# Optimization experiments

Measured on AMD Instinct MI355X. Metric: run time of the kernel, lower is better.

The kernel has to match this reference:

```python
import jax, jax.numpy as jnp
import numpy as np

N, E, D = 20000, 320000, 256
EPS = 1e-5


def setup_inputs() -> dict:
    key = jax.random.key(0)
    ks = jax.random.split(key, 12)
    s = 1.0 / np.sqrt(D)
    s2 = 1.0 / np.sqrt(2 * D)
    return {
        "node_embeddings": jax.random.normal(ks[0], (N, D), jnp.float32),
        "edge_index": jax.random.randint(ks[1], (2, E), 0, N, jnp.int64),
        "edge_embeddings": jax.random.normal(ks[2], (E, D), jnp.float32),
        # message MLP: Linear(D,D) -> GELU -> Linear(D,D)
        "W1m": jax.random.uniform(ks[3], (D, D), jnp.float32, -s, s),
        "b1m": jnp.zeros((D,), jnp.float32),
        "W2m": jax.random.uniform(ks[4], (D, D), jnp.float32, -s, s),
        "b2m": jnp.zeros((D,), jnp.float32),
        # update MLP: Linear(D,2D) -> GELU -> Linear(2D,D)
        "W1u": jax.random.uniform(ks[5], (D, 2 * D), jnp.float32, -s, s),
        "b1u": jnp.zeros((2 * D,), jnp.float32),
        "W2u": jax.random.uniform(ks[6], (2 * D, D), jnp.float32, -s2, s2),
        "b2u": jnp.zeros((D,), jnp.float32),
        # LayerNorm params
        "gamma": jnp.ones((D,), jnp.float32),
        "beta": jnp.zeros((D,), jnp.float32),
    }


def _layer_norm(x, gamma, beta):
    mu = jnp.mean(x, axis=-1, keepdims=True)
    var = jnp.mean(jnp.square(x - mu), axis=-1, keepdims=True)
    return (x - mu) * jax.lax.rsqrt(var + EPS) * gamma + beta


def reference(node_embeddings, edge_index, edge_embeddings,
              W1m, b1m, W2m, b2m, W1u, b1u, W2u, b2u, gamma, beta):
    src = edge_index[0]
    dst = edge_index[1]
    n = node_embeddings.shape[0]
    # gather + edge add + message MLP (exact erf GELU, as torch default)
    h = node_embeddings[src] + edge_embeddings           # [E, D]
    h = jax.nn.gelu(h @ W1m + b1m, approximate=False)
    messages = h @ W2m + b2m                             # [E, D]
    # scatter-mean aggregation
    agg = jax.ops.segment_sum(messages, dst, num_segments=n)  # [N, D]
    deg = jax.ops.segment_sum(jnp.ones((dst.shape[0], 1), node_embeddings.dtype),
                              dst, num_segments=n)            # [N, 1]
    agg = agg / jnp.maximum(deg, 1.0)
    # update MLP + residual + LayerNorm
    u = jax.nn.gelu(agg @ W1u + b1u, approximate=False) @ W2u + b2u
    return _layer_norm(node_embeddings + u, gamma, beta)
```

## Files before the change

kernel.cpp:

```cpp
#include <hip/hip_runtime.h>
#include <hip/hip_bf16.h>

#define N_NODES 20000
#define N_EDGES 320000
#define EBLK 32
#define NBLK 32

typedef __attribute__((ext_vector_type(8))) short short8;
typedef __attribute__((ext_vector_type(4))) float f32x4;

static __device__ __forceinline__ unsigned short f2bf(float f) {
  __hip_bfloat16 h = __float2bfloat16(f);
  union { __hip_bfloat16 h; unsigned short u; } cv; cv.h = h; return cv.u;
}

static __device__ __forceinline__ unsigned int pk2(float a, float b) {
  return (unsigned int)f2bf(a) | ((unsigned int)f2bf(b) << 16);
}

static __device__ __forceinline__ float gelu_f(float x) {
  float z = x * (2.3022082f + 0.1029432f * x * x);
  z = fminf(fmaxf(z, -30.0f), 30.0f);
  float t = exp2f(z);
  return x * t * __frcp_rn(1.0f + t);
}

#define SWZ(row, byteoff) ((byteoff) ^ (((row) & 7) << 4))
#define SWZU(b) ((b) ^ ((((b) >> 8) & 7) << 4))

__global__ void zero_kernel(float4* __restrict__ S4, int4* __restrict__ cnt4) {
  int idx = blockIdx.x * blockDim.x + threadIdx.x;
  S4[idx] = make_float4(0.f, 0.f, 0.f, 0.f);
  if (idx < N_NODES / 4) cnt4[idx] = make_int4(0, 0, 0, 0);
}

__global__ void pack_kernel(const float* __restrict__ W1m, const float* __restrict__ W2m,
                            const float* __restrict__ W1u, const float* __restrict__ W2u,
                            unsigned short* __restrict__ P1m, unsigned short* __restrict__ P2m,
                            unsigned short* __restrict__ P1u, unsigned short* __restrict__ P2u) {
  int idx = blockIdx.x * blockDim.x + threadIdx.x;
  const float* W; unsigned short* P; int K, Nc, local;
  if (idx < 65536)        { W = W1m; P = P1m; K = 256; Nc = 256; local = idx; }
  else if (idx < 131072)  { W = W2m; P = P2m; K = 256; Nc = 256; local = idx - 65536; }
  else if (idx < 262144)  { W = W1u; P = P1u; K = 256; Nc = 512; local = idx - 131072; }
  else                    { W = W2u; P = P2u; K = 512; Nc = 256; local = idx - 262144; }
  int frag = local >> 9, wi = local & 511;
  int l = wi >> 3, i = wi & 7;
  int kf = K >> 5;
  int cf = frag / kf, t = frag % kf;
  int k = t * 32 + (l >> 4) * 8 + i;
  int n = cf * 16 + (l & 15);
  P[local] = f2bf(W[(size_t)k * Nc + n]);
}

__global__ void hist_kernel(const int* __restrict__ dst, int* __restrict__ cnt) {
  int e = blockIdx.x * blockDim.x + threadIdx.x;
  atomicAdd(&cnt[dst[e]], 1);
}

__global__ __launch_bounds__(1024) void scan_kernel(const int* __restrict__ cnt,
                                                    int* __restrict__ rptr,
                                                    int* __restrict__ cur) {
  __shared__ int sums[1024];
  const int t = threadIdx.x;
  const int base = t * 20;
  int local[20];
  int s = 0;
#pragma unroll
  for (int i = 0; i < 20; ++i) {
    int idx = base + i;
    int v = (idx < N_NODES) ? cnt[idx] : 0;
    local[i] = s;
    s += v;
  }
  int v = s;
  sums[t] = v;
  for (int off = 1; off < 1024; off <<= 1) {
    __syncthreads();
    int o = (t >= off) ? sums[t - off] : 0;
    __syncthreads();
    v += o;
    sums[t] = v;
  }
  int excl = v - s;
#pragma unroll
  for (int i = 0; i < 20; ++i) {
    int idx = base + i;
    if (idx < N_NODES) { int p = excl + local[i]; rptr[idx] = p; cur[idx] = p; }
  }
  if (t == 1023) rptr[N_NODES] = v;
}

__global__ void scatter_kernel(const int* __restrict__ dst, int* __restrict__ cur,
                               int* __restrict__ perm) {
  int e = blockIdx.x * blockDim.x + threadIdx.x;
  int d = dst[e];
  int pos = atomicAdd(&cur[d], 1);
  perm[pos] = e;
}

__global__ __launch_bounds__(256, 8) void edge_kernel(
    const float* __restrict__ node, const float* __restrict__ eemb,
    const int* __restrict__ src, const int* __restrict__ dst,
    const int* __restrict__ perm,
    const unsigned short* __restrict__ P1m, const float* __restrict__ b1m,
    float* __restrict__ S) {
  __shared__ unsigned short tA[EBLK * 256];
  __shared__ int dstS[EBLK];
  const int tid = threadIdx.x;
  const int e0 = blockIdx.x * EBLK;
  {
    const int r = tid >> 3;
    const int cs = (tid & 7) * 32;
    const int e = perm[e0 + r];
    const int se = src[e];
    if ((tid & 7) == 0) dstS[r] = dst[e];
    const float* ep = eemb + (size_t)e * 256 + cs;
    const float* np = node + (size_t)se * 256 + cs;
#pragma unroll
    for (int i = 0; i < 4; ++i) {
      float4 a = *(const float4*)(ep + i * 8);
      float4 b = *(const float4*)(np + i * 8);
      float4 c = *(const float4*)(ep + i * 8 + 4);
      float4 d = *(const float4*)(np + i * 8 + 4);
      uint4 p;
      p.x = pk2(a.x + b.x, a.y + b.y);
      p.y = pk2(a.z + b.z, a.w + b.w);
      p.z = pk2(c.x + d.x, c.y + d.y);
      p.w = pk2(c.z + d.z, c.w + d.w);
      *(uint4*)((char*)tA + SWZ(r, r * 512 + (cs + i * 8) * 2)) = p;
    }
  }
  __syncthreads();

  const int w = tid >> 6, l = tid & 63;
  const int lr = l & 15, lh = l >> 4;
  f32x4 acc[2][4];
#pragma unroll
  for (int c = 0; c < 4; ++c) {
    float bb = b1m[w * 64 + c * 16 + lr];
    acc[0][c] = f32x4{bb, bb, bb, bb};
    acc[1][c] = f32x4{bb, bb, bb, bb};
  }
#pragma unroll
  for (int kt = 0; kt < 8; ++kt) {
    const int row0 = lr, row1 = 16 + lr;
    short8 af0 = *(const short8*)((const char*)tA + SWZ(row0, row0 * 512 + kt * 64 + lh * 16));
    short8 af1 = *(const short8*)((const char*)tA + SWZ(row1, row1 * 512 + kt * 64 + lh * 16));
#pragma unroll
    for (int c = 0; c < 4; ++c) {
      short8 bfr = *(const short8*)(P1m + (size_t)(((w * 4 + c) * 8 + kt) * 512 + l * 8));
      acc[0][c] = __builtin_amdgcn_mfma_f32_16x16x32_bf16(af0, bfr, acc[0][c], 0, 0, 0);
      acc[1][c] = __builtin_amdgcn_mfma_f32_16x16x32_bf16(af1, bfr, acc[1][c], 0, 0, 0);
    }
  }

#pragma unroll
  for (int r4 = 0; r4 < 2; ++r4)
#pragma unroll
    for (int c = 0; c < 4; ++c)
#pragma unroll
      for (int j = 0; j < 4; ++j)
        acc[r4][c][j] = gelu_f(acc[r4][c][j]);

  const int dv = dstS[l & 31];
  const int pv = __shfl(dv, (l - 1) & 63);
  const bool bflag = (l < 32) && ((l == 0) || (dv != pv));
  const unsigned long long mask = __ballot(bflag);
  const int nseg = __popcll(mask);
  int sid[2][4];
#pragma unroll
  for (int r4 = 0; r4 < 2; ++r4)
#pragma unroll
    for (int j = 0; j < 4; ++j) {
      int row = r4 * 16 + lh * 4 + j;
      sid[r4][j] = __popcll(mask & ((2ULL << row) - 1)) - 1;
    }
  unsigned long long rem = mask;
  for (int s = 0; s < nseg; ++s) {
    const int rowf = __builtin_ctzll(rem);
    rem &= rem - 1;
    const int dseg = __shfl(dv, rowf);
    float p0 = 0.f, p1 = 0.f, p2 = 0.f, p3 = 0.f;
#pragma unroll
    for (int r4 = 0; r4 < 2; ++r4)
#pragma unroll
      for (int j = 0; j < 4; ++j) {
        bool m = (sid[r4][j] == s);
        p0 += m ? acc[r4][0][j] : 0.f;
        p1 += m ? acc[r4][1][j] : 0.f;
        p2 += m ? acc[r4][2][j] : 0.f;
        p3 += m ? acc[r4][3][j] : 0.f;
      }
    p0 += __shfl_xor(p0, 16); p0 += __shfl_xor(p0, 32);
    p1 += __shfl_xor(p1, 16); p1 += __shfl_xor(p1, 32);
    p2 += __shfl_xor(p2, 16); p2 += __shfl_xor(p2, 32);
    p3 += __shfl_xor(p3, 16); p3 += __shfl_xor(p3, 32);
    if (lh == 0) {
      float* Sp = S + (size_t)dseg * 256 + w * 64 + lr;
      atomicAdd(Sp, p0);
      atomicAdd(Sp + 16, p1);
      atomicAdd(Sp + 32, p2);
      atomicAdd(Sp + 48, p3);
    }
  }
}

__global__ __launch_bounds__(256, 4) void node_kernel(
    const float* __restrict__ node, const float* __restrict__ S, const int* __restrict__ rptr,
    const unsigned short* __restrict__ P2m, const float* __restrict__ b2m,
    const unsigned short* __restrict__ P1u, const float* __restrict__ b1u,
    const unsigned short* __restrict__ P2u, const float* __restrict__ b2u,
    const float* __restrict__ gamma, const float* __restrict__ beta,
    float* __restrict__ out) {
  __shared__ unsigned short tAB[2][NBLK * 256];
  __shared__ unsigned short tH[NBLK * 256];
  __shared__ float fmu[NBLK], frs[NBLK], fflag[NBLK];
  float* tU = (float*)tAB;
  const int tid = threadIdx.x;
  const int n0 = blockIdx.x * NBLK;
  const int r = tid >> 3;
  const int cs = (tid & 7) * 32;
  const int n = n0 + r;
  {
    int dgi = rptr[n + 1] - rptr[n];
    float rec = 1.0f / fmaxf((float)dgi, 1.0f);
    if ((tid & 7) == 0) fflag[r] = (dgi > 0) ? 1.0f : 0.0f;
    const float* sp = S + (size_t)n * 256 + cs;
#pragma unroll
    for (int i = 0; i < 4; ++i) {
      float4 a = *(const float4*)(sp + i * 8);
      float4 b = *(const float4*)(sp + i * 8 + 4);
      uint4 p;
      p.x = pk2(a.x * rec, a.y * rec);
      p.y = pk2(a.z * rec, a.w * rec);
      p.z = pk2(b.x * rec, b.y * rec);
      p.w = pk2(b.z * rec, b.w * rec);
      *(uint4*)((char*)tAB[0] + SWZ(r, r * 512 + (cs + i * 8) * 2)) = p;
    }
  }
  __syncthreads();
  const int w = tid >> 6, l = tid & 63, lr = l & 15, lh = l >> 4;

  {
    f32x4 acc[2][4];
#pragma unroll
    for (int r4 = 0; r4 < 2; ++r4)
#pragma unroll
      for (int c = 0; c < 4; ++c) acc[r4][c] = f32x4{0.f, 0.f, 0.f, 0.f};
#pragma unroll
    for (int t = 0; t < 8; ++t) {
      const int row0 = lr, row1 = 16 + lr;
      short8 af0 = *(const short8*)((const char*)tAB[0] + SWZ(row0, row0 * 512 + t * 64 + lh * 16));
      short8 af1 = *(const short8*)((const char*)tAB[0] + SWZ(row1, row1 * 512 + t * 64 + lh * 16));
#pragma unroll
      for (int c = 0; c < 4; ++c) {
        short8 bfr = *(const short8*)(P2m + (size_t)(((w * 4 + c) * 8 + t) * 512 + l * 8));
        acc[0][c] = __builtin_amdgcn_mfma_f32_16x16x32_bf16(af0, bfr, acc[0][c], 0, 0, 0);
        acc[1][c] = __builtin_amdgcn_mfma_f32_16x16x32_bf16(af1, bfr, acc[1][c], 0, 0, 0);
      }
    }
#pragma unroll
    for (int r4 = 0; r4 < 2; ++r4)
#pragma unroll
      for (int c = 0; c < 4; ++c) {
        int col = w * 64 + c * 16 + lr;
        float bm = b2m[col];
#pragma unroll
        for (int j = 0; j < 4; ++j) {
          int row = r4 * 16 + lh * 4 + j;
          float v = acc[r4][c][j] + fflag[row] * bm;
          *(unsigned short*)((char*)tAB[1] + SWZ(row, row * 512 + col * 2)) = f2bf(v);
        }
      }
  }
  __syncthreads();

  f32x4 acc3[2][4];
#pragma unroll
  for (int c = 0; c < 4; ++c) {
    float bb = b2u[w * 64 + c * 16 + lr];
    acc3[0][c] = f32x4{bb, bb, bb, bb};
    acc3[1][c] = f32x4{bb, bb, bb, bb};
  }
#pragma unroll
  for (int half = 0; half < 2; ++half) {
    {
      f32x4 acc[2][4];
#pragma unroll
      for (int r4 = 0; r4 < 2; ++r4)
#pragma unroll
        for (int c = 0; c < 4; ++c) acc[r4][c] = f32x4{0.f, 0.f, 0.f, 0.f};
#pragma unroll
      for (int t = 0; t < 8; ++t) {
        const int row0 = lr, row1 = 16 + lr;
        short8 af0 = *(const short8*)((const char*)tAB[1] + SWZ(row0, row0 * 512 + t * 64 + lh * 16));
        short8 af1 = *(const short8*)((const char*)tAB[1] + SWZ(row1, row1 * 512 + t * 64 + lh * 16));
#pragma unroll
        for (int c = 0; c < 4; ++c) {
          short8 bfr = *(const short8*)(P1u + (size_t)(((half * 16 + w * 4 + c) * 8 + t) * 512 + l * 8));
          acc[0][c] = __builtin_amdgcn_mfma_f32_16x16x32_bf16(af0, bfr, acc[0][c], 0, 0, 0);
          acc[1][c] = __builtin_amdgcn_mfma_f32_16x16x32_bf16(af1, bfr, acc[1][c], 0, 0, 0);
        }
      }
#pragma unroll
      for (int r4 = 0; r4 < 2; ++r4)
#pragma unroll
        for (int c = 0; c < 4; ++c) {
          int col = w * 64 + c * 16 + lr;
          float b1 = b1u[half * 256 + col];
#pragma unroll
          for (int j = 0; j < 4; ++j) {
            int row = r4 * 16 + lh * 4 + j;
            float v = gelu_f(acc[r4][c][j] + b1);
            *(unsigned short*)((char*)tH + SWZ(row, row * 512 + col * 2)) = f2bf(v);
          }
        }
    }
    __syncthreads();
    {
#pragma unroll
      for (int tt = 0; tt < 8; ++tt) {
        const int row0 = lr, row1 = 16 + lr;
        short8 af0 = *(const short8*)((const char*)tH + SWZ(row0, row0 * 512 + tt * 64 + lh * 16));
        short8 af1 = *(const short8*)((const char*)tH + SWZ(row1, row1 * 512 + tt * 64 + lh * 16));
#pragma unroll
        for (int c = 0; c < 4; ++c) {
          short8 bfr = *(const short8*)(P2u + (size_t)(((w * 4 + c) * 16 + half * 8 + tt) * 512 + l * 8));
          acc3[0][c] = __builtin_amdgcn_mfma_f32_16x16x32_bf16(af0, bfr, acc3[0][c], 0, 0, 0);
          acc3[1][c] = __builtin_amdgcn_mfma_f32_16x16x32_bf16(af1, bfr, acc3[1][c], 0, 0, 0);
        }
      }
    }
    __syncthreads();
  }

#pragma unroll
  for (int r4 = 0; r4 < 2; ++r4)
#pragma unroll
    for (int c = 0; c < 4; ++c) {
      int col = w * 64 + c * 16 + lr;
#pragma unroll
      for (int j = 0; j < 4; ++j) {
        int row = r4 * 16 + lh * 4 + j;
        *(float*)((char*)tU + SWZU(row * 1024 + col * 4)) = acc3[r4][c][j];
      }
    }
  __syncthreads();

  {
    float sum = 0.f, sq = 0.f;
#pragma unroll
    for (int i = 0; i < 8; ++i) {
      int byte = SWZU(r * 1024 + (cs + i * 4) * 4);
      float4 v = *(float4*)((char*)tU + byte);
      const float4 nb = *(const float4*)(node + (size_t)n * 256 + cs + i * 4);
      v.x += nb.x; v.y += nb.y; v.z += nb.z; v.w += nb.w;
      *(float4*)((char*)tU + byte) = v;
      sum += v.x + v.y + v.z + v.w;
      sq += v.x * v.x + v.y * v.y + v.z * v.z + v.w * v.w;
    }
    sum += __shfl_xor(sum, 1); sum += __shfl_xor(sum, 2); sum += __shfl_xor(sum, 4);
    sq  += __shfl_xor(sq, 1);  sq  += __shfl_xor(sq, 2);  sq  += __shfl_xor(sq, 4);
    if ((tid & 7) == 0) {
      float mu = sum * (1.0f / 256.0f);
      fmu[r] = mu;
      frs[r] = rsqrtf(fmaxf(sq * (1.0f / 256.0f) - mu * mu, 0.0f) + 1e-5f);
    }
  }
  __syncthreads();
#pragma unroll
  for (int i = 0; i < 8; ++i) {
    int f4 = i * 256 + tid;
    int row = f4 >> 6;
    int c4 = f4 & 63;
    float4 v = *(float4*)((char*)tU + SWZU(row * 1024 + c4 * 16));
    float mu = fmu[row], rs = frs[row];
    float4 g  = *(const float4*)(gamma + c4 * 4);
    float4 bt = *(const float4*)(beta + c4 * 4);
    float4 o;
    o.x = (v.x - mu) * rs * g.x + bt.x;
    o.y = (v.y - mu) * rs * g.y + bt.y;
    o.z = (v.z - mu) * rs * g.z + bt.z;
    o.w = (v.w - mu) * rs * g.w + bt.w;
    *(float4*)(out + (size_t)(n0 + row) * 256 + c4 * 4) = o;
  }
}

extern "C" void kernel_launch(void* const* d_in, const int* in_sizes, int n_in,
                              void* d_out, int out_size, void* d_ws, size_t ws_size,
                              hipStream_t stream) {
  const float* node = (const float*)d_in[0];
  const int* eidx = (const int*)d_in[1];
  const float* eemb = (const float*)d_in[2];
  const float* W1m = (const float*)d_in[3];
  const float* b1m = (const float*)d_in[4];
  const float* W2m = (const float*)d_in[5];
  const float* b2m = (const float*)d_in[6];
  const float* W1u = (const float*)d_in[7];
  const float* b1u = (const float*)d_in[8];
  const float* W2u = (const float*)d_in[9];
  const float* b2u = (const float*)d_in[10];
  const float* gamma = (const float*)d_in[11];
  const float* beta = (const float*)d_in[12];
  float* out = (float*)d_out;

  char* ws = (char*)d_ws;
  int* cnt  = (int*)ws;
  int* rptr = (int*)(ws + 81920);
  int* cur  = (int*)(ws + 163840);
  int* perm = (int*)(ws + 245760);
  unsigned short* P1m = (unsigned short*)(ws + 1525760);
  unsigned short* P2m = (unsigned short*)(ws + 1656832);
  unsigned short* P1u = (unsigned short*)(ws + 1787904);
  unsigned short* P2u = (unsigned short*)(ws + 2050048);
  const int* src = eidx;
  const int* dst = eidx + N_EDGES;

  zero_kernel<<<N_NODES * 64 / 256, 256, 0, stream>>>((float4*)out, (int4*)cnt);
  pack_kernel<<<393216 / 256, 256, 0, stream>>>(W1m, W2m, W1u, W2u, P1m, P2m, P1u, P2u);
  hist_kernel<<<N_EDGES / 256, 256, 0, stream>>>(dst, cnt);
  scan_kernel<<<1, 1024, 0, stream>>>(cnt, rptr, cur);
  scatter_kernel<<<N_EDGES / 256, 256, 0, stream>>>(dst, cur, perm);
  edge_kernel<<<N_EDGES / EBLK, 256, 0, stream>>>(node, eemb, src, dst, perm, P1m, b1m, out);
  node_kernel<<<N_NODES / NBLK, 256, 0, stream>>>(node, out, rptr, P2m, b2m,
                                                  P1u, b1u, P2u, b2u, gamma, beta, out);
}
```

Measured before the change: 374.5 us.

## Tile edge kernel over 64 edges with 512 threads and fuse init kernels

Each edge_kernel block now handles 64 edges with 8 waves instead of 32 edges with 4. Each wave computes 32 output columns over four 16-row tiles, so each B-fragment load from the packed weights is reused across more rows. The segmented scatter now reduces over 64-row segments, which is meant to cut the number of global atomics at block boundaries. The zero and weight-pack kernels are merged into one launch. Higher per-thread accumulator and fragment register use combined with launch_bounds(512,8) could cause spills or lower occupancy.

```diff
diff --git a/kernel.cpp b/kernel.cpp
--- a/kernel.cpp
+++ b/kernel.cpp
@@ -3,7 +3,7 @@
 
 #define N_NODES 20000
 #define N_EDGES 320000
-#define EBLK 32
+#define EBLK 64
 #define NBLK 32
 
 typedef __attribute__((ext_vector_type(8))) short short8;
@@ -28,17 +28,19 @@
 #define SWZ(row, byteoff) ((byteoff) ^ (((row) & 7) << 4))
 #define SWZU(b) ((b) ^ ((((b) >> 8) & 7) << 4))
 
-__global__ void zero_kernel(float4* __restrict__ S4, int4* __restrict__ cnt4) {
-  int idx = blockIdx.x * blockDim.x + threadIdx.x;
-  S4[idx] = make_float4(0.f, 0.f, 0.f, 0.f);
-  if (idx < N_NODES / 4) cnt4[idx] = make_int4(0, 0, 0, 0);
-}
-
-__global__ void pack_kernel(const float* __restrict__ W1m, const float* __restrict__ W2m,
+__global__ void init_kernel(float4* __restrict__ S4, int4* __restrict__ cnt4,
+                            const float* __restrict__ W1m, const float* __restrict__ W2m,
                             const float* __restrict__ W1u, const float* __restrict__ W2u,
                             unsigned short* __restrict__ P1m, unsigned short* __restrict__ P2m,
                             unsigned short* __restrict__ P1u, unsigned short* __restrict__ P2u) {
-  int idx = blockIdx.x * blockDim.x + threadIdx.x;
+  const int b = blockIdx.x;
+  if (b < 5000) {
+    int idx = b * blockDim.x + threadIdx.x;
+    S4[idx] = make_float4(0.f, 0.f, 0.f, 0.f);
+    if (idx < N_NODES / 4) cnt4[idx] = make_int4(0, 0, 0, 0);
+    return;
+  }
+  int idx = (b - 5000) * blockDim.x + threadIdx.x;
   const float* W; unsigned short* P; int K, Nc, local;
   if (idx < 65536)        { W = W1m; P = P1m; K = 256; Nc = 256; local = idx; }
   else if (idx < 131072)  { W = W2m; P = P2m; K = 256; Nc = 256; local = idx - 65536; }
@@ -99,7 +101,7 @@
   perm[pos] = e;
 }
 
-__global__ __launch_bounds__(256, 8) void edge_kernel(
+__global__ __launch_bounds__(512, 8) void edge_kernel(
     const float* __restrict__ node, const float* __restrict__ eemb,
     const int* __restrict__ src, const int* __restrict__ dst,
     const int* __restrict__ perm,
@@ -135,42 +137,46 @@
 
   const int w = tid >> 6, l = tid & 63;
   const int lr = l & 15, lh = l >> 4;
-  f32x4 acc[2][4];
-#pragma unroll
-  for (int c = 0; c < 4; ++c) {
-    float bb = b1m[w * 64 + c * 16 + lr];
-    acc[0][c] = f32x4{bb, bb, bb, bb};
-    acc[1][c] = f32x4{bb, bb, bb, bb};
+  f32x4 acc[4][2];
+#pragma unroll
+  for (int c = 0; c < 2; ++c) {
+    float bb = b1m[w * 32 + c * 16 + lr];
+#pragma unroll
+    for (int r4 = 0; r4 < 4; ++r4) acc[r4][c] = f32x4{bb, bb, bb, bb};
   }
 #pragma unroll
   for (int kt = 0; kt < 8; ++kt) {
-    const int row0 = lr, row1 = 16 + lr;
-    short8 af0 = *(const short8*)((const char*)tA + SWZ(row0, row0 * 512 + kt * 64 + lh * 16));
-    short8 af1 = *(const short8*)((const char*)tA + SWZ(row1, row1 * 512 + kt * 64 + lh * 16));
-#pragma unroll
-    for (int c = 0; c < 4; ++c) {
-      short8 bfr = *(const short8*)(P1m + (size_t)(((w * 4 + c) * 8 + kt) * 512 + l * 8));
-      acc[0][c] = __builtin_amdgcn_mfma_f32_16x16x32_bf16(af0, bfr, acc[0][c], 0, 0, 0);
-      acc[1][c] = __builtin_amdgcn_mfma_f32_16x16x32_bf16(af1, bfr, acc[1][c], 0, 0, 0);
-    }
-  }
-
-#pragma unroll
-  for (int r4 = 0; r4 < 2; ++r4)
-#pragma unroll
-    for (int c = 0; c < 4; ++c)
+    short8 af[4];
+#pragma unroll
+    for (int r4 = 0; r4 < 4; ++r4) {
+      int row = r4 * 16 + lr;
+      af[r4] = *(const short8*)((const char*)tA + SWZ(row, row * 512 + kt * 64 + lh * 16));
+    }
+#pragma unroll
+    for (int c = 0; c < 2; ++c) {
+      short8 bfr = *(const short8*)(P1m + (size_t)(((w * 2 + c) * 8 + kt) * 512 + l * 8));
+#pragma unroll
+      for (int r4 = 0; r4 < 4; ++r4)
+        acc[r4][c] = __builtin_amdgcn_mfma_f32_16x16x32_bf16(af[r4], bfr, acc[r4][c], 0, 0, 0);
+    }
+  }
+
+#pragma unroll
+  for (int r4 = 0; r4 < 4; ++r4)
+#pragma unroll
+    for (int c = 0; c < 2; ++c)
 #pragma unroll
       for (int j = 0; j < 4; ++j)
         acc[r4][c][j] = gelu_f(acc[r4][c][j]);
 
-  const int dv = dstS[l & 31];
+  const int dv = dstS[l];
   const int pv = __shfl(dv, (l - 1) & 63);
-  const bool bflag = (l < 32) && ((l == 0) || (dv != pv));
+  const bool bflag = (l == 0) || (dv != pv);
   const unsigned long long mask = __ballot(bflag);
   const int nseg = __popcll(mask);
-  int sid[2][4];
-#pragma unroll
-  for (int r4 = 0; r4 < 2; ++r4)
+  int sid[4][4];
+#pragma unroll
+  for (int r4 = 0; r4 < 4; ++r4)
 #pragma unroll
     for (int j = 0; j < 4; ++j) {
       int row = r4 * 16 + lh * 4 + j;
@@ -181,27 +187,21 @@
     const int rowf = __builtin_ctzll(rem);
     rem &= rem - 1;
     const int dseg = __shfl(dv, rowf);
-    float p0 = 0.f, p1 = 0.f, p2 = 0.f, p3 = 0.f;
-#pragma unroll
-    for (int r4 = 0; r4 < 2; ++r4)
+    float p0 = 0.f, p1 = 0.f;
+#pragma unroll
+    for (int r4 = 0; r4 < 4; ++r4)
 #pragma unroll
       for (int j = 0; j < 4; ++j) {
         bool m = (sid[r4][j] == s);
         p0 += m ? acc[r4][0][j] : 0.f;
         p1 += m ? acc[r4][1][j] : 0.f;
-        p2 += m ? acc[r4][2][j] : 0.f;
-        p3 += m ? acc[r4][3][j] : 0.f;
       }
     p0 += __shfl_xor(p0, 16); p0 += __shfl_xor(p0, 32);
     p1 += __shfl_xor(p1, 16); p1 += __shfl_xor(p1, 32);
-    p2 += __shfl_xor(p2, 16); p2 += __shfl_xor(p2, 32);
-    p3 += __shfl_xor(p3, 16); p3 += __shfl_xor(p3, 32);
     if (lh == 0) {
-      float* Sp = S + (size_t)dseg * 256 + w * 64 + lr;
+      float* Sp = S + (size_t)dseg * 256 + w * 32 + lr;
       atomicAdd(Sp, p0);
       atomicAdd(Sp + 16, p1);
-      atomicAdd(Sp + 32, p2);
-      atomicAdd(Sp + 48, p3);
     }
   }
 }
@@ -417,12 +417,12 @@
   const int* src = eidx;
   const int* dst = eidx + N_EDGES;
 
-  zero_kernel<<<N_NODES * 64 / 256, 256, 0, stream>>>((float4*)out, (int4*)cnt);
-  pack_kernel<<<393216 / 256, 256, 0, stream>>>(W1m, W2m, W1u, W2u, P1m, P2m, P1u, P2u);
+  init_kernel<<<5000 + 1536, 256, 0, stream>>>((float4*)out, (int4*)cnt,
+                                               W1m, W2m, W1u, W2u, P1m, P2m, P1u, P2u);
   hist_kernel<<<N_EDGES / 256, 256, 0, stream>>>(dst, cnt);
   scan_kernel<<<1, 1024, 0, stream>>>(cnt, rptr, cur);
   scatter_kernel<<<N_EDGES / 256, 256, 0, stream>>>(dst, cur, perm);
-  edge_kernel<<<N_EDGES / EBLK, 256, 0, stream>>>(node, eemb, src, dst, perm, P1m, b1m, out);
+  edge_kernel<<<N_EDGES / EBLK, 512, 0, stream>>>(node, eemb, src, dst, perm, P1m, b1m, out);
   node_kernel<<<N_NODES / NBLK, 256, 0, stream>>>(node, out, rptr, P2m, b2m,
                                                   P1u, b1u, P2u, b2u, gamma, beta, out);
 }
```

Measured after the change: 348.6 us. 6.9% less time.
